# Kernel optimization log

Measured on AMD Instinct MI355X. Metric: run time of the kernel, lower is better.

## Reference

```python
import jax, jax.numpy as jnp
import numpy as np

LN_EPS = 1e-5  # torch nn.LayerNorm default


def setup_inputs() -> dict:
    key = jax.random.key(0)
    kx, kw = jax.random.split(key)
    tokens, d_in, d_out = 8192, 4096, 16384
    x = jax.random.normal(kx, (tokens, d_in), dtype=jnp.float32)
    # nn.Linear weight layout: [out_features, in_features]
    W = jax.random.normal(kw, (d_out, d_in), dtype=jnp.float32) * (1.0 / np.sqrt(d_in))
    return {"x": x, "W": W}


def reference(x, W):
    # LayerNorm over last dim, no affine params (elementwise_affine=False)
    mean = jnp.mean(x, axis=-1, keepdims=True)
    var = jnp.mean(jnp.square(x - mean), axis=-1, keepdims=True)  # biased, as torch LN
    xn = (x - mean) * jax.lax.rsqrt(var + LN_EPS)
    # Linear (no bias): [tokens, d_in] @ [d_in, d_out]
    y = jnp.einsum("td,od->to", xn, W)
    return jax.nn.sigmoid(y)
```

## Files before the change

kernel.cpp:

```cpp
#include <hip/hip_runtime.h>
#include <hip/hip_bf16.h>
#include <stdint.h>

#define TOKENS 8192
#define DIN    4096
#define DOUT   16384

#define BM 256
#define BN 256
#define BKT 64
#define NT (DIN / BKT)
#define NJ (NT / 2)

typedef short s16x8 __attribute__((ext_vector_type(8)));
typedef float f32x16 __attribute__((ext_vector_type(16)));

#define AS1 __attribute__((address_space(1)))
#define AS3 __attribute__((address_space(3)))
#define VMCNT(n)  asm volatile("s_waitcnt vmcnt(" #n ")" ::: "memory")
#define BAR()     __builtin_amdgcn_s_barrier()

__device__ __forceinline__ unsigned short f2bf(float f) {
  unsigned int u = __float_as_uint(f);
  u += 0x7fffu + ((u >> 16) & 1u);
  return (unsigned short)(u >> 16);
}

__global__ __launch_bounds__(256) void ln_kernel(const float* __restrict__ x,
                                                 unsigned short* __restrict__ xn) {
  const int row = blockIdx.x;
  const float4* xr = reinterpret_cast<const float4*>(x + (size_t)row * DIN);
  float4 v[4];
  float sum = 0.f, ssq = 0.f;
#pragma unroll
  for (int i = 0; i < 4; ++i) {
    v[i] = xr[threadIdx.x + i * 256];
    sum += v[i].x + v[i].y + v[i].z + v[i].w;
    ssq += v[i].x * v[i].x + v[i].y * v[i].y + v[i].z * v[i].z + v[i].w * v[i].w;
  }
#pragma unroll
  for (int off = 32; off > 0; off >>= 1) {
    sum += __shfl_xor(sum, off, 64);
    ssq += __shfl_xor(ssq, off, 64);
  }
  __shared__ float red[8];
  const int wid = threadIdx.x >> 6;
  if ((threadIdx.x & 63) == 0) { red[wid] = sum; red[wid + 4] = ssq; }
  __syncthreads();
  sum = red[0] + red[1] + red[2] + red[3];
  ssq = red[4] + red[5] + red[6] + red[7];
  const float mean = sum * (1.f / DIN);
  const float var  = ssq * (1.f / DIN) - mean * mean;
  const float rs   = rsqrtf(var + 1e-5f);
  ushort4* xo = reinterpret_cast<ushort4*>(xn + (size_t)row * DIN);
#pragma unroll
  for (int i = 0; i < 4; ++i) {
    ushort4 o;
    o.x = f2bf((v[i].x - mean) * rs);
    o.y = f2bf((v[i].y - mean) * rs);
    o.z = f2bf((v[i].z - mean) * rs);
    o.w = f2bf((v[i].w - mean) * rs);
    xo[threadIdx.x + i * 256] = o;
  }
}

__global__ __launch_bounds__(256) void cvt_kernel(const float* __restrict__ W,
                                                  unsigned short* __restrict__ Wb) {
  const size_t i = (size_t)blockIdx.x * 256 + threadIdx.x;
  float4 v = reinterpret_cast<const float4*>(W)[i];
  ushort4 o;
  o.x = f2bf(v.x); o.y = f2bf(v.y); o.z = f2bf(v.z); o.w = f2bf(v.w);
  reinterpret_cast<ushort4*>(Wb)[i] = o;
}

__global__ __launch_bounds__(512, 2) void gemm_sig(const unsigned short* __restrict__ A,
                                                   const unsigned short* __restrict__ B,
                                                   float* __restrict__ C) {
  __shared__ unsigned short Asl[2 * 256 * 64];
  __shared__ unsigned short Bsl[2 * 256 * 64];

  const int bid = blockIdx.x;
  const int cpx = gridDim.x >> 3;
  const int swz = (bid & 7) * cpx + (bid >> 3);
  const int grp = swz >> 2;
  const int sub = swz & 3;
  const int bm = ((grp & 15) << 1) | (sub & 1);
  const int bn = ((grp >> 4) << 1) | (sub >> 1);

  const int tid  = threadIdx.x;
  const int wid  = tid >> 6;
  const int lane = tid & 63;
  const int wr = wid >> 2, wc = wid & 3;

  const unsigned short* gA = A + (size_t)bm * BM * DIN;
  const unsigned short* gB = B + (size_t)bn * BN * DIN;

  const int l8 = lane >> 3, l7 = lane & 7;
  const int csw = l7 ^ l8;
  const unsigned short* sA = gA + (size_t)(wid * 8 + l8) * DIN + csw * 8;
  const unsigned short* sB = gB + (size_t)(wid * 8 + l8) * DIN + csw * 8;
  const int dOfs = wid * 512;

#define STG_A(p, kt) do { _Pragma("unroll") for (int q = 0; q < 4; ++q) \
  __builtin_amdgcn_global_load_lds( \
    (const AS1 void*)(sA + (size_t)q * 64 * DIN + (size_t)(kt) * BKT), \
    (AS3 void*)(Asl + ((p) * 256 + q * 64) * 64 + dOfs), 16, 0, 0); } while (0)
#define STG_B(p, kt) do { _Pragma("unroll") for (int q = 0; q < 4; ++q) \
  __builtin_amdgcn_global_load_lds( \
    (const AS1 void*)(sB + (size_t)q * 64 * DIN + (size_t)(kt) * BKT), \
    (AS3 void*)(Bsl + ((p) * 256 + q * 64) * 64 + dOfs), 16, 0, 0); } while (0)

  const int l31 = lane & 31;
  const int l5  = lane >> 5;
  int aRow[4], bRow[2], kslt[4];
#pragma unroll
  for (int mb = 0; mb < 4; ++mb) aRow[mb] = (wr * 128 + mb * 32 + l31) * 64;
#pragma unroll
  for (int nb = 0; nb < 2; ++nb) bRow[nb] = (wc * 64 + nb * 32 + l31) * 64;
#pragma unroll
  for (int ks = 0; ks < 4; ++ks) kslt[ks] = ((2 * ks + l5) ^ l7) * 8;

  s16x8 a0[4], a1[4], bX[8], bY[8];
  f32x16 acc[4][2] = {};

#define RD_AP(p, mp) do { _Pragma("unroll") for (int ks = 0; ks < 4; ++ks) { \
    a0[ks] = *reinterpret_cast<const s16x8*>(Asl + (p) * 16384 + aRow[2 * (mp)] + kslt[ks]); \
    a1[ks] = *reinterpret_cast<const s16x8*>(Asl + (p) * 16384 + aRow[2 * (mp) + 1] + kslt[ks]); } } while (0)
#define RD_BPRE(p, dst) do { _Pragma("unroll") for (int ks = 0; ks < 4; ++ks) { \
    dst[ks]     = *reinterpret_cast<const s16x8*>(Bsl + (p) * 16384 + bRow[0] + kslt[ks]); \
    dst[4 + ks] = *reinterpret_cast<const s16x8*>(Bsl + (p) * 16384 + bRow[1] + kslt[ks]); } } while (0)
#define MMPH(mp, bArr) do { _Pragma("unroll") for (int ks = 0; ks < 4; ++ks) { \
    acc[2 * (mp)][0]     = __builtin_amdgcn_mfma_f32_32x32x16_bf16(a0[ks], bArr[ks],     acc[2 * (mp)][0], 0, 0, 0); \
    acc[2 * (mp)][1]     = __builtin_amdgcn_mfma_f32_32x32x16_bf16(a0[ks], bArr[4 + ks], acc[2 * (mp)][1], 0, 0, 0); \
    acc[2 * (mp) + 1][0] = __builtin_amdgcn_mfma_f32_32x32x16_bf16(a1[ks], bArr[ks],     acc[2 * (mp) + 1][0], 0, 0, 0); \
    acc[2 * (mp) + 1][1] = __builtin_amdgcn_mfma_f32_32x32x16_bf16(a1[ks], bArr[4 + ks], acc[2 * (mp) + 1][1], 0, 0, 0); } } while (0)

  STG_B(0, 0); STG_A(0, 0); STG_B(1, 1);
  VMCNT(4); BAR();
  RD_BPRE(0, bX);

  for (int j = 0; j < NJ - 1; ++j) {
    const int t1 = 2 * j + 1, t2 = 2 * j + 2, t3 = 2 * j + 3;
    VMCNT(4);
    RD_AP(0, 0);
    STG_A(1, t1);
    MMPH(0, bX); BAR();
    VMCNT(4);
    RD_AP(0, 1); RD_BPRE(1, bY);
    STG_B(0, t2);
    MMPH(1, bX); BAR();
    VMCNT(4);
    RD_AP(1, 0);
    STG_A(0, t2);
    MMPH(0, bY); BAR();
    VMCNT(4);
    RD_AP(1, 1); RD_BPRE(0, bX);
    STG_B(1, t3);
    MMPH(1, bY); BAR();
  }

  {
    const int t1 = NT - 1;
    VMCNT(4);
    RD_AP(0, 0);
    STG_A(1, t1);
    MMPH(0, bX); BAR();
    VMCNT(4);
    RD_AP(0, 1); RD_BPRE(1, bY);
    MMPH(1, bX); BAR();
    VMCNT(0);
    RD_AP(1, 0);
    MMPH(0, bY); BAR();
    RD_AP(1, 1);
    MMPH(1, bY); BAR();
  }

#undef STG_A
#undef STG_B
#undef RD_AP
#undef RD_BPRE
#undef MMPH

  const int crow0 = bm * BM + wr * 128 + 4 * l5;
  const int ccol0 = bn * BN + wc * 64 + l31;
#pragma unroll
  for (int mb = 0; mb < 4; ++mb)
#pragma unroll
    for (int nb = 0; nb < 2; ++nb)
#pragma unroll
      for (int reg = 0; reg < 16; ++reg) {
        const int r = crow0 + mb * 32 + (reg & 3) + 8 * (reg >> 2);
        const int c = ccol0 + nb * 32;
        const float v = acc[mb][nb][reg];
        C[(size_t)r * DOUT + c] = 1.f / (1.f + __expf(-v));
      }
}

extern "C" void kernel_launch(void* const* d_in, const int* in_sizes, int n_in,
                              void* d_out, int out_size, void* d_ws, size_t ws_size,
                              hipStream_t stream) {
  const float* x = (const float*)d_in[0];
  const float* W = (const float*)d_in[1];
  float* out = (float*)d_out;

  unsigned short* xn = (unsigned short*)d_ws;
  unsigned short* Wb = xn + (size_t)TOKENS * DIN;

  ln_kernel<<<TOKENS, 256, 0, stream>>>(x, xn);
  cvt_kernel<<<((size_t)DOUT * DIN) / 1024, 256, 0, stream>>>(W, Wb);
  gemm_sig<<<(TOKENS / BM) * (DOUT / BN), 512, 0, stream>>>(xn, Wb, out);
}
```

Measured before the change: 1.155 ms.

## Restructure GEMM main loop with double-buffered A fragments and merged tail

Reworks the software pipeline of the bf16 MFMA GEMM. A fragments now double-buffer in registers (aX/aY), so both M-halves of a tile are read from LDS before compute. The global-to-LDS staging order and vmcnt waits change, including a full vmcnt(0) wait at the start of each iteration. The separate epilogue is folded into the loop with a last-iteration guard. This is meant to improve overlap between LDS reads, global loads and MFMAs. It adds register pressure under the 2-wave occupancy bound, and the stricter waits may expose load latency.

```diff
diff --git a/kernel.cpp b/kernel.cpp
--- a/kernel.cpp
+++ b/kernel.cpp
@@ -120,59 +120,43 @@
 #pragma unroll
   for (int ks = 0; ks < 4; ++ks) kslt[ks] = ((2 * ks + l5) ^ l7) * 8;
 
-  s16x8 a0[4], a1[4], bX[8], bY[8];
+  s16x8 aX[8], aY[8], bX[8], bY[8];
   f32x16 acc[4][2] = {};
 
-#define RD_AP(p, mp) do { _Pragma("unroll") for (int ks = 0; ks < 4; ++ks) { \
-    a0[ks] = *reinterpret_cast<const s16x8*>(Asl + (p) * 16384 + aRow[2 * (mp)] + kslt[ks]); \
-    a1[ks] = *reinterpret_cast<const s16x8*>(Asl + (p) * 16384 + aRow[2 * (mp) + 1] + kslt[ks]); } } while (0)
+#define RD_AP(p, mp, dst) do { _Pragma("unroll") for (int ks = 0; ks < 4; ++ks) { \
+    dst[ks]     = *reinterpret_cast<const s16x8*>(Asl + (p) * 16384 + aRow[2 * (mp)] + kslt[ks]); \
+    dst[4 + ks] = *reinterpret_cast<const s16x8*>(Asl + (p) * 16384 + aRow[2 * (mp) + 1] + kslt[ks]); } } while (0)
 #define RD_BPRE(p, dst) do { _Pragma("unroll") for (int ks = 0; ks < 4; ++ks) { \
     dst[ks]     = *reinterpret_cast<const s16x8*>(Bsl + (p) * 16384 + bRow[0] + kslt[ks]); \
     dst[4 + ks] = *reinterpret_cast<const s16x8*>(Bsl + (p) * 16384 + bRow[1] + kslt[ks]); } } while (0)
-#define MMPH(mp, bArr) do { _Pragma("unroll") for (int ks = 0; ks < 4; ++ks) { \
-    acc[2 * (mp)][0]     = __builtin_amdgcn_mfma_f32_32x32x16_bf16(a0[ks], bArr[ks],     acc[2 * (mp)][0], 0, 0, 0); \
-    acc[2 * (mp)][1]     = __builtin_amdgcn_mfma_f32_32x32x16_bf16(a0[ks], bArr[4 + ks], acc[2 * (mp)][1], 0, 0, 0); \
-    acc[2 * (mp) + 1][0] = __builtin_amdgcn_mfma_f32_32x32x16_bf16(a1[ks], bArr[ks],     acc[2 * (mp) + 1][0], 0, 0, 0); \
-    acc[2 * (mp) + 1][1] = __builtin_amdgcn_mfma_f32_32x32x16_bf16(a1[ks], bArr[4 + ks], acc[2 * (mp) + 1][1], 0, 0, 0); } } while (0)
+#define MMPH(mp, aArr, bArr) do { _Pragma("unroll") for (int ks = 0; ks < 4; ++ks) { \
+    acc[2 * (mp)][0]     = __builtin_amdgcn_mfma_f32_32x32x16_bf16(aArr[ks],     bArr[ks],     acc[2 * (mp)][0], 0, 0, 0); \
+    acc[2 * (mp)][1]     = __builtin_amdgcn_mfma_f32_32x32x16_bf16(aArr[ks],     bArr[4 + ks], acc[2 * (mp)][1], 0, 0, 0); \
+    acc[2 * (mp) + 1][0] = __builtin_amdgcn_mfma_f32_32x32x16_bf16(aArr[4 + ks], bArr[ks],     acc[2 * (mp) + 1][0], 0, 0, 0); \
+    acc[2 * (mp) + 1][1] = __builtin_amdgcn_mfma_f32_32x32x16_bf16(aArr[4 + ks], bArr[4 + ks], acc[2 * (mp) + 1][1], 0, 0, 0); } } while (0)
 
-  STG_B(0, 0); STG_A(0, 0); STG_B(1, 1);
-  VMCNT(4); BAR();
+  STG_A(0, 0); STG_B(0, 0);
+  STG_A(1, 1); STG_B(1, 1);
+  VMCNT(8); BAR();
   RD_BPRE(0, bX);
 
-  for (int j = 0; j < NJ - 1; ++j) {
-    const int t1 = 2 * j + 1, t2 = 2 * j + 2, t3 = 2 * j + 3;
+  for (int j = 0; j < NJ; ++j) {
+    const int t2 = 2 * j + 2, t3 = 2 * j + 3;
+    const bool last = (j == NJ - 1);
+    VMCNT(0);
+    RD_AP(0, 0, aX); RD_AP(0, 1, aY);
+    if (!last) STG_B(0, t2);
+    MMPH(0, aX, bX); BAR();
+    RD_AP(1, 0, aX); RD_BPRE(1, bY);
+    if (!last) STG_A(0, t2);
+    MMPH(1, aY, bX); BAR();
     VMCNT(4);
-    RD_AP(0, 0);
-    STG_A(1, t1);
-    MMPH(0, bX); BAR();
+    RD_AP(1, 1, aY);
+    if (!last) STG_B(1, t3);
+    MMPH(0, aX, bY); BAR();
     VMCNT(4);
-    RD_AP(0, 1); RD_BPRE(1, bY);
-    STG_B(0, t2);
-    MMPH(1, bX); BAR();
-    VMCNT(4);
-    RD_AP(1, 0);
-    STG_A(0, t2);
-    MMPH(0, bY); BAR();
-    VMCNT(4);
-    RD_AP(1, 1); RD_BPRE(0, bX);
-    STG_B(1, t3);
-    MMPH(1, bY); BAR();
-  }
-
-  {
-    const int t1 = NT - 1;
-    VMCNT(4);
-    RD_AP(0, 0);
-    STG_A(1, t1);
-    MMPH(0, bX); BAR();
-    VMCNT(4);
-    RD_AP(0, 1); RD_BPRE(1, bY);
-    MMPH(1, bX); BAR();
-    VMCNT(0);
-    RD_AP(1, 0);
-    MMPH(0, bY); BAR();
-    RD_AP(1, 1);
-    MMPH(1, bY); BAR();
+    if (!last) { RD_BPRE(0, bX); STG_A(1, t3); }
+    MMPH(1, aY, bY); BAR();
   }
 
 #undef STG_A
```

Measured after the change: 1.160 ms. No clear change (+0.4%).
